# Performance work log

Measured on AMD Instinct MI355X. Metric: run time of the kernel, lower is better.

The kernel has to match this reference:

```python
import math
import jax, jax.numpy as jnp
import numpy as np

N_HEADS = 16
HIDDEN = 1024
FACTOR = 256
N_DK = HIDDEN // N_HEADS
B, S = 4, 2048


def _linear_params(key, fan_in, fan_out):
    kw, kb = jax.random.split(key)
    bound = 1.0 / math.sqrt(fan_in)
    W = jax.random.uniform(kw, (fan_in, fan_out), jnp.float32, -bound, bound)
    b = jax.random.uniform(kb, (fan_out,), jnp.float32, -bound, bound)
    return W, b


def setup_inputs() -> dict:
    key = jax.random.key(0)
    ks = jax.random.split(key, 12)
    inp = {
        "query": jax.random.normal(ks[0], (B, S, HIDDEN), jnp.float32),
        "key": jax.random.normal(ks[1], (B, S, HIDDEN), jnp.float32),
        "value": jax.random.normal(ks[2], (B, S, HIDDEN), jnp.float32),
        "mask": jax.random.randint(ks[3], (B, S), 0, 2, jnp.int32),
    }
    names = [("pq", HIDDEN, FACTOR), ("tq", FACTOR, HIDDEN),
             ("pk", HIDDEN, FACTOR), ("tk", FACTOR, HIDDEN),
             ("pv", HIDDEN, FACTOR), ("tv", FACTOR, HIDDEN),
             ("po", HIDDEN, FACTOR), ("to", FACTOR, HIDDEN)]
    for i, (nm, fi, fo) in enumerate(names):
        W, b = _linear_params(ks[4 + i], fi, fo)
        inp[f"W{nm}"], inp[f"b{nm}"] = W, b
    return inp


def _factored(x, Wp, bp, Wt, bt):
    # proj -> leaky_relu(0.2) -> tran
    h = jax.nn.leaky_relu(x @ Wp + bp, negative_slope=0.2)
    return h @ Wt + bt


def reference(query, key, value, mask,
              Wpq, bpq, Wtq, btq, Wpk, bpk, Wtk, btk,
              Wpv, bpv, Wtv, btv, Wpo, bpo, Wto, bto):
    bsize = query.shape[0]

    def split_heads(x):  # [B,S,H*Dk] -> [B,H,S,Dk]
        return x.reshape(bsize, -1, N_HEADS, N_DK).transpose(0, 2, 1, 3)

    q = split_heads(_factored(query, Wpq, bpq, Wtq, btq))
    k = split_heads(_factored(key, Wpk, bpk, Wtk, btk))
    v = split_heads(_factored(value, Wpv, bpv, Wtv, btv))

    scores = jnp.einsum("bhqd,bhkd->bhqk", q, k) / math.sqrt(N_DK)
    m = (mask == 0)[:, None, None, :]  # [B,1,1,S]
    scores = jnp.where(m, jnp.float32(-1e20), scores)
    attn = jax.nn.softmax(scores, axis=-1)
    cv = jnp.einsum("bhqk,bhkd->bhqd", attn, v)
    cv = cv.transpose(0, 2, 1, 3).reshape(bsize, -1, N_HEADS * N_DK)
    # dropout omitted (eval mode / deterministic reference)
    return _factored(cv, Wpo, bpo, Wto, bto)
```

## Files before the change

### kernel.cpp

```cpp
#include <hip/hip_runtime.h>
#include <cstdint>
#include <cstddef>

typedef __bf16 bf16_t;
typedef __bf16 bf16x8 __attribute__((ext_vector_type(8)));
typedef float  f32x4  __attribute__((ext_vector_type(4)));
typedef unsigned int uint32x4 __attribute__((ext_vector_type(4)));
typedef unsigned int uint32x2 __attribute__((ext_vector_type(2)));

#define DEV_INLINE __device__ __forceinline__

constexpr int Bsz = 4, Ssz = 2048, HID = 1024, FAC = 256, NH = 16, DKc = 64;
constexpr int Mrows = Bsz * Ssz;
constexpr float QSCALE = 0.18033688011112042f;

struct Ptr8 { const float* p[8]; };
struct Ptr3 { const float* p[3]; };

DEV_INLINE float fast_exp2(float x) {
#if __has_builtin(__builtin_amdgcn_exp2f)
  return __builtin_amdgcn_exp2f(x);
#else
  return exp2f(x);
#endif
}

DEV_INLINE void async16(const void* g, void* l) {
  __builtin_amdgcn_global_load_lds((const __attribute__((address_space(1))) void*)g,
                                   (__attribute__((address_space(3))) void*)l, 16, 0, 0);
}

#define WBAR(N) do { \
  asm volatile("s_waitcnt vmcnt(" #N ") lgkmcnt(0)" ::: "memory"); \
  __builtin_amdgcn_s_barrier(); \
} while (0)

DEV_INLINE int SW(int r) { return (r & 3) | ((r >> 1) & 4); }
DEV_INLINE int SW32(int r) { return (r >> 1) & 3; }

__global__ __launch_bounds__(256) void k_prep(Ptr8 w, Ptr8 bsrc, const int* __restrict__ mask,
                                              bf16_t* wpt, bf16_t* wtt,
                                              float* bp, float* bt, float* mf, bf16_t* mb) {
  const int z = blockIdx.z;
  if (z == 8) {
    if (blockIdx.x >= 64) return;
    const int i = blockIdx.x * 256 + threadIdx.x;
    if (i < 4 * FAC) bp[i] = bsrc.p[i >> 8][i & 255];
    if (i < 4 * HID) bt[i] = bsrc.p[4 + (i >> 10)][i & 1023];
    if (i < Bsz * Ssz) {
      const float m = (mask[i] != 0) ? 1.f : 0.f;
      mf[i] = m;
      mb[i] = (bf16_t)m;
    }
    return;
  }
  const int K = (z < 4) ? HID : FAC;
  const int N = (z < 4) ? FAC : HID;
  const int nbN = N / 32;
  const int nb = (blockIdx.x % nbN) * 32, kb = (blockIdx.x / nbN) * 32;
  __shared__ float t[32][33];
  const float* src = w.p[z];
  bf16_t* dst = (z < 4) ? (wpt + (size_t)z * FAC * HID) : (wtt + (size_t)(z - 4) * FAC * HID);
  const int tx = threadIdx.x & 31, ty = threadIdx.x >> 5;
#pragma unroll
  for (int j = 0; j < 4; ++j)
    t[ty + j * 8][tx] = src[(size_t)(kb + ty + j * 8) * N + nb + tx];
  __syncthreads();
#pragma unroll
  for (int j = 0; j < 4; ++j)
    dst[(size_t)(nb + ty + j * 8) * K + kb + tx] = (bf16_t)t[tx][ty + j * 8];
}

template <int CAST_A, int QKV, typename OUT_T>
__global__ __launch_bounds__(512, 2) void k_fact2(Ptr3 Asrc, const bf16_t* __restrict__ Abf,
                                                  const bf16_t* __restrict__ WpB,
                                                  const float* __restrict__ bpB,
                                                  const bf16_t* __restrict__ WtB,
                                                  const float* __restrict__ btB,
                                                  OUT_T* __restrict__ CoutAll,
                                                  bf16_t* __restrict__ C2,
                                                  const float* __restrict__ rowmul) {
  constexpr int LDTA = CAST_A ? 40 : 32;
  __shared__ __align__(16) bf16_t smem[128 * 264 + 4 * 256 * 32];
  bf16_t* As = smem;
  bf16_t* Hl = smem;
  bf16_t* Bs = smem + 128 * 264;

  const int z = QKV ? blockIdx.z : 0;
  const bf16_t* Wp = WpB + (size_t)z * FAC * HID;
  const float* bp = bpB + z * FAC;
  const bf16_t* Wt = WtB + (size_t)z * FAC * HID;
  const float* bt = btB + z * HID;
  OUT_T* Cout = QKV ? (CoutAll + (size_t)z * Mrows * HID) : CoutAll;

  const int tid = threadIdx.x;
  const int lane = tid & 63, wave = tid >> 6;
  const int quad = lane >> 4, l16 = lane & 15;
  const int swl = SW32(l16);
  const int m0 = blockIdx.x * 128;

  const int b1row = wave * 32 + (lane >> 2);
  const int bslot = (((lane & 3) ^ SW32(b1row)) & 3) * 8;
  const int wOff = wave * 1024;
  const bf16_t* gW0 = Wp + (size_t)b1row * HID + bslot;
  const bf16_t* gW1 = gW0 + (size_t)16 * HID;

  const int crow = tid >> 2, chalf = (tid & 3) * 8;
  const float* gAf = nullptr;
  const bf16_t* gAb = nullptr;
  if (CAST_A) {
    gAf = Asrc.p[z] + (size_t)(m0 + crow) * HID + chalf;
  } else {
    const int arowA = wave * 16 + (lane >> 2);
    const int aslot = (((lane & 3) ^ SW32(arowA)) & 3) * 8;
    gAb = Abf + (size_t)(m0 + arowA) * HID + aslot;
  }

#define STB1(t)                                              \
  do {                                                       \
    const int k0_ = (t) * 32;                                \
    bf16_t* d_ = Bs + ((t) & 3) * 8192 + wOff;               \
    async16(gW0 + k0_, d_);                                  \
    async16(gW1 + k0_, d_ + 512);                            \
  } while (0)
#define STA1(t) async16(gAb + (t) * 32, As + ((t) & 3) * 4096 + wave * 512)

  if (CAST_A) {
    f32x4 pa = *(const f32x4*)gAf;
    f32x4 pb = *(const f32x4*)(gAf + 4);
    __builtin_amdgcn_sched_barrier(0);
    STB1(0);
    STB1(1);
    union { bf16_t h[8]; uint32x4 u; } o;
#pragma unroll
    for (int j = 0; j < 4; ++j) { o.h[j] = (bf16_t)pa[j]; o.h[4 + j] = (bf16_t)pb[j]; }
    *(uint32x4*)(As + crow * LDTA + chalf) = o.u;
  } else {
    STA1(0); STB1(0);
    STA1(1); STB1(1);
  }

  f32x4 acc[8][2] = {};
  constexpr int nk = 32;

  for (int it = 0; it < nk; ++it) {
    if (CAST_A) {
      f32x4 xa, xb;
      const int k1 = (it + 1) * 32;
      if (it + 1 < nk) {
        xa = *(const f32x4*)(gAf + k1);
        xb = *(const f32x4*)(gAf + k1 + 4);
      }
      __builtin_amdgcn_sched_barrier(0);
      if (it + 2 < nk) STB1(it + 2);
      if (it + 2 < nk)      WBAR(6);
      else if (it + 1 < nk) WBAR(4);
      else                  WBAR(0);

      const bf16_t* Ac = As + (it % 3) * (128 * 40);
      const bf16_t* Bc = Bs + (it & 3) * 8192;
      bf16x8 af[8], bfr[2];
#pragma unroll
      for (int i = 0; i < 8; ++i)
        af[i] = *(const bf16x8*)(Ac + (i * 16 + l16) * LDTA + quad * 8);
#pragma unroll
      for (int i = 0; i < 2; ++i)
        bfr[i] = *(const bf16x8*)(Bc + (wave * 32 + i * 16 + l16) * 32 + ((quad ^ swl) & 3) * 8);
#pragma unroll
      for (int mi = 0; mi < 8; ++mi)
#pragma unroll
        for (int ni = 0; ni < 2; ++ni)
          acc[mi][ni] = __builtin_amdgcn_mfma_f32_16x16x32_bf16(af[mi], bfr[ni], acc[mi][ni], 0, 0, 0);

      if (it + 1 < nk) {
        union { bf16_t h[8]; uint32x4 u; } o;
#pragma unroll
        for (int j = 0; j < 4; ++j) { o.h[j] = (bf16_t)xa[j]; o.h[4 + j] = (bf16_t)xb[j]; }
        *(uint32x4*)(As + ((it + 1) % 3) * (128 * 40) + crow * LDTA + chalf) = o.u;
      }
    } else {
      if (it + 2 < nk) { STA1(it + 2); STB1(it + 2); }
      if (it + 2 < nk)      WBAR(6);
      else if (it + 1 < nk) WBAR(3);
      else                  WBAR(0);

      const bf16_t* Ac = As + (it & 3) * 4096;
      const bf16_t* Bc = Bs + (it & 3) * 8192;
      bf16x8 af[8], bfr[2];
#pragma unroll
      for (int i = 0; i < 8; ++i)
        af[i] = *(const bf16x8*)(Ac + (i * 16 + l16) * LDTA + ((quad ^ swl) & 3) * 8);
#pragma unroll
      for (int i = 0; i < 2; ++i)
        bfr[i] = *(const bf16x8*)(Bc + (wave * 32 + i * 16 + l16) * 32 + ((quad ^ swl) & 3) * 8);
#pragma unroll
      for (int mi = 0; mi < 8; ++mi)
#pragma unroll
        for (int ni = 0; ni < 2; ++ni)
          acc[mi][ni] = __builtin_amdgcn_mfma_f32_16x16x32_bf16(af[mi], bfr[ni], acc[mi][ni], 0, 0, 0);
    }
  }
#undef STA1

  __syncthreads();
#pragma unroll
  for (int mi = 0; mi < 8; ++mi)
#pragma unroll
    for (int ni = 0; ni < 2; ++ni) {
      const int col = wave * 32 + ni * 16 + l16;
      const float bv = bp[col];
#pragma unroll
      for (int r = 0; r < 4; ++r) {
        float y = acc[mi][ni][r] + bv;
        y = (y > 0.f) ? y : 0.2f * y;
        Hl[(mi * 16 + quad * 4 + r) * 264 + col] = (bf16_t)y;
      }
      acc[mi][ni] = (f32x4){0.f, 0.f, 0.f, 0.f};
    }
  __syncthreads();

#define STG2(ci)                                                              \
  do {                                                                        \
    const int nb_ = ((ci) >> 3) * 256, k0_ = ((ci) & 7) * 32;                 \
    const bf16_t* g_ = Wt + (size_t)(nb_ + b1row) * FAC + k0_ + bslot;        \
    bf16_t* d_ = Bs + ((ci) & 3) * 8192 + wOff;                               \
    async16(g_, d_);                                                          \
    async16(g_ + 16 * FAC, d_ + 512);                                         \
  } while (0)

  STG2(0);
  STG2(1);

  for (int ci = 0; ci < 32; ++ci) {
    if (ci + 2 < 32) STG2(ci + 2);
    if (ci + 2 < 32)      WBAR(4);
    else if (ci + 1 < 32) WBAR(2);
    else                  WBAR(0);

    const bf16_t* Bc = Bs + (ci & 3) * 8192;
    const int k0 = (ci & 7) * 32;
    bf16x8 af[8], bfr[2];
#pragma unroll
    for (int i = 0; i < 8; ++i)
      af[i] = *(const bf16x8*)(Hl + (i * 16 + l16) * 264 + k0 + quad * 8);
#pragma unroll
    for (int i = 0; i < 2; ++i)
      bfr[i] = *(const bf16x8*)(Bc + (wave * 32 + i * 16 + l16) * 32 + ((quad ^ swl) & 3) * 8);
#pragma unroll
    for (int mi = 0; mi < 8; ++mi)
#pragma unroll
      for (int ni = 0; ni < 2; ++ni)
        acc[mi][ni] = __builtin_amdgcn_mfma_f32_16x16x32_bf16(af[mi], bfr[ni], acc[mi][ni], 0, 0, 0);

    if ((ci & 7) == 7) {
      const int nbase = (ci >> 3) * 256;
      if (QKV && z == 2) {
#pragma unroll
        for (int mi = 0; mi < 8; ++mi) {
          const int rbase = m0 + mi * 16 + quad * 4;
          const int bb = rbase >> 11, s = rbase & 2047;
          float rmv[4];
#pragma unroll
          for (int r = 0; r < 4; ++r) rmv[r] = rowmul[rbase + r];
#pragma unroll
          for (int ni = 0; ni < 2; ++ni) {
            const int col = nbase + wave * 32 + ni * 16 + l16;
            const float bv = bt[col];
            const int hh = col >> 6, d = col & 63;
            union { bf16_t e[4]; uint32x2 u; } p;
#pragma unroll
            for (int r = 0; r < 4; ++r) p.e[r] = (bf16_t)((acc[mi][ni][r] + bv) * rmv[r]);
            *(uint32x2*)(C2 + (((size_t)((bb * NH + hh) * DKc + d)) << 11) + s) = p.u;
          }
        }
      } else {
        const float scale = (QKV && z == 0) ? QSCALE : 1.f;
#pragma unroll
        for (int mi = 0; mi < 8; ++mi) {
          const int row = m0 + mi * 16 + quad * 4;
#pragma unroll
          for (int ni = 0; ni < 2; ++ni) {
            const int col = nbase + wave * 32 + ni * 16 + l16;
            const float bv = bt[col];
#pragma unroll
            for (int r = 0; r < 4; ++r)
              Cout[(size_t)(row + r) * HID + col] = (OUT_T)((acc[mi][ni][r] + bv) * scale);
          }
        }
      }
#pragma unroll
      for (int mi = 0; mi < 8; ++mi)
#pragma unroll
        for (int ni = 0; ni < 2; ++ni) acc[mi][ni] = (f32x4){0.f, 0.f, 0.f, 0.f};
    }
  }
#undef STG2
#undef STB1
}

__global__ __launch_bounds__(512, 2) void k_attn(const bf16_t* __restrict__ qkv,
                                                 const bf16_t* __restrict__ mb,
                                                 bf16_t* __restrict__ cv) {
  __shared__ __align__(16) bf16_t Ks[4][64 * 64];
  __shared__ __align__(16) bf16_t Vt[4][64 * 64];
  __shared__ __align__(16) bf16_t Ml[Ssz];

  const int qt = blockIdx.x, h = blockIdx.y, b = blockIdx.z;
  const bf16_t* qp = qkv;
  const bf16_t* kp = qkv + (size_t)Mrows * HID;
  const bf16_t* vtp = qkv + 2 * (size_t)Mrows * HID + (size_t)(b * NH + h) * DKc * Ssz;

  const int tid = threadIdx.x;
  const int lane = tid & 63, wave = tid >> 6;
  const int quad = lane >> 4, l16 = lane & 15;

  const int r0 = wave * 8 + (lane >> 3);
  const int c0 = ((lane & 7) ^ SW(r0)) * 8;
  const int ldsOff = wave * 512;
  const bf16_t* kgA = kp + (size_t)(b * Ssz + r0) * HID + h * DKc + c0;
  const bf16_t* vgA = vtp + (size_t)r0 * Ssz + c0;

#define STAGEA(t, buf)                                          \
  do {                                                          \
    async16(kgA + (size_t)(t) * 64 * HID, Ks[buf] + ldsOff);    \
    async16(vgA + (t) * 64, Vt[buf] + ldsOff);                  \
  } while (0)

  *(uint32x2*)(Ml + tid * 4) = *(const uint32x2*)(mb + (size_t)b * Ssz + tid * 4);
  STAGEA(0, 0);
  STAGEA(1, 1);

  bf16x8 aq0[4], aq1[4];
#pragma unroll
  for (int g = 0; g < 4; ++g) {
    const size_t qrow = (size_t)(b * Ssz + qt * 512 + g * 128 + wave * 16 + l16) * HID + h * DKc + quad * 8;
    aq0[g] = *(const bf16x8*)(qp + qrow);
    aq1[g] = *(const bf16x8*)(qp + qrow + 32);
  }

  const int krow = 8 * (l16 >> 2) + (l16 & 3);
  f32x4 acc[4][4] = {};
  f32x4 dacc[4] = {};
  const bf16x8 zfrag = {};

  for (int kt = 0; kt < 32; ++kt) {
    if (kt + 2 < 32) STAGEA(kt + 2, (kt + 2) & 3);

    if (kt + 2 < 32)      WBAR(4);
    else if (kt + 1 < 32) WBAR(2);
    else                  WBAR(0);

    const bf16_t* Kc = Ks[kt & 3];
    const bf16_t* Vc = Vt[kt & 3];

    union U { uint32x4 u; bf16x8 h; } ap0[4], ap1[4];
    constexpr int koff[4] = {0, 4, 32, 36};
#pragma unroll
    for (int ks = 0; ks < 4; ++ks) {
      const int row = krow + koff[ks];
      const int sw = SW(row);
      bf16x8 a0 = *(const bf16x8*)(Kc + row * 64 + (quad ^ sw) * 8);
      bf16x8 a1 = *(const bf16x8*)(Kc + row * 64 + ((quad + 4) ^ sw) * 8);
#pragma unroll
      for (int g = 0; g < 4; ++g) {
        f32x4 c = {};
        c = __builtin_amdgcn_mfma_f32_16x16x32_bf16(a0, aq0[g], c, 0, 0, 0);
        c = __builtin_amdgcn_mfma_f32_16x16x32_bf16(a1, aq1[g], c, 0, 0, 0);
        union { bf16_t h[2]; uint32_t u; } p01, p23;
        p01.h[0] = (bf16_t)fast_exp2(c[0]);
        p01.h[1] = (bf16_t)fast_exp2(c[1]);
        p23.h[0] = (bf16_t)fast_exp2(c[2]);
        p23.h[1] = (bf16_t)fast_exp2(c[3]);
        U& t = (ks < 2) ? ap0[g] : ap1[g];
        t.u[(ks & 1) * 2] = p01.u;
        t.u[(ks & 1) * 2 + 1] = p23.u;
      }
    }

    bf16x8 mr0 = *(const bf16x8*)(Ml + kt * 64 + quad * 8);
    bf16x8 mr1 = *(const bf16x8*)(Ml + kt * 64 + 32 + quad * 8);
    if (l16 != 0) { mr0 = zfrag; mr1 = zfrag; }
#pragma unroll
    for (int g = 0; g < 4; ++g) {
      dacc[g] = __builtin_amdgcn_mfma_f32_16x16x32_bf16(ap0[g].h, mr0, dacc[g], 0, 0, 0);
      dacc[g] = __builtin_amdgcn_mfma_f32_16x16x32_bf16(ap1[g].h, mr1, dacc[g], 0, 0, 0);
    }

#pragma unroll
    for (int d = 0; d < 4; ++d) {
      const int row = d * 16 + l16;
      const int sw = SW(row);
      bf16x8 bv0 = *(const bf16x8*)(Vc + row * 64 + (quad ^ sw) * 8);
      bf16x8 bv1 = *(const bf16x8*)(Vc + row * 64 + ((quad + 4) ^ sw) * 8);
#pragma unroll
      for (int g = 0; g < 4; ++g) {
        acc[g][d] = __builtin_amdgcn_mfma_f32_16x16x32_bf16(ap0[g].h, bv0, acc[g][d], 0, 0, 0);
        acc[g][d] = __builtin_amdgcn_mfma_f32_16x16x32_bf16(ap1[g].h, bv1, acc[g][d], 0, 0, 0);
      }
    }
  }
#undef STAGEA

#pragma unroll
  for (int g = 0; g < 4; ++g) {
    const size_t obase = (size_t)(b * Ssz + qt * 512 + g * 128 + wave * 16 + quad * 4) * HID + h * DKc + l16;
#pragma unroll
    for (int r = 0; r < 4; ++r) {
      const float denom = __shfl(dacc[g][r], lane & 48, 64);
      const float rl = 1.f / denom;
#pragma unroll
      for (int d = 0; d < 4; ++d)
        cv[obase + (size_t)r * HID + d * 16] = (bf16_t)(acc[g][d][r] * rl);
    }
  }
}

extern "C" void kernel_launch(void* const* d_in, const int* in_sizes, int n_in,
                              void* d_out, int out_size, void* d_ws, size_t ws_size,
                              hipStream_t stream) {
  (void)in_sizes; (void)n_in; (void)out_size; (void)ws_size;
  const float* q_in = (const float*)d_in[0];
  const float* k_in = (const float*)d_in[1];
  const float* v_in = (const float*)d_in[2];
  const int* mask = (const int*)d_in[3];

  bf16_t* XB = (bf16_t*)d_ws;
  bf16_t* H3 = XB + (size_t)3 * Mrows * HID;
  bf16_t* CV = H3 + (size_t)3 * Mrows * FAC;
  bf16_t* WPT = CV + (size_t)Mrows * HID;
  bf16_t* WTT = WPT + (size_t)4 * FAC * HID;
  float* BP = (float*)(WTT + (size_t)4 * FAC * HID);
  float* BT = BP + 4 * FAC;
  float* MF = BT + 4 * HID;
  bf16_t* MB = (bf16_t*)(MF + Mrows);
  bf16_t* VTg = XB + 2 * (size_t)Mrows * HID;

  Ptr8 w;
  w.p[0] = (const float*)d_in[4];  w.p[1] = (const float*)d_in[8];
  w.p[2] = (const float*)d_in[12]; w.p[3] = (const float*)d_in[16];
  w.p[4] = (const float*)d_in[6];  w.p[5] = (const float*)d_in[10];
  w.p[6] = (const float*)d_in[14]; w.p[7] = (const float*)d_in[18];
  Ptr8 bs;
  bs.p[0] = (const float*)d_in[5];  bs.p[1] = (const float*)d_in[9];
  bs.p[2] = (const float*)d_in[13]; bs.p[3] = (const float*)d_in[17];
  bs.p[4] = (const float*)d_in[7];  bs.p[5] = (const float*)d_in[11];
  bs.p[6] = (const float*)d_in[15]; bs.p[7] = (const float*)d_in[19];
  hipLaunchKernelGGL(k_prep, dim3(256, 1, 9), dim3(256), 0, stream, w, bs, mask,
                     WPT, WTT, BP, BT, MF, MB);

  Ptr3 xs; xs.p[0] = q_in; xs.p[1] = k_in; xs.p[2] = v_in;
  Ptr3 nullp; nullp.p[0] = nullp.p[1] = nullp.p[2] = nullptr;

  hipLaunchKernelGGL((k_fact2<1, 1, bf16_t>), dim3(Mrows / 128, 1, 3), dim3(512), 0, stream,
                     xs, (const bf16_t*)nullptr, WPT, BP, WTT, BT, XB, VTg, MF);

  hipLaunchKernelGGL(k_attn, dim3(Ssz / 512, NH, Bsz), dim3(512), 0, stream, XB, MB, CV);

  hipLaunchKernelGGL((k_fact2<0, 0, float>), dim3(Mrows / 128, 1, 1), dim3(512), 0, stream,
                     nullp, CV, WPT + (size_t)3 * FAC * HID, BP + 3 * FAC,
                     WTT + (size_t)3 * FAC * HID, BT + 3 * HID,
                     (float*)d_out, (bf16_t*)nullptr, (const float*)nullptr);
}
```

Measured before the change: 332.8 us.

## Load GEMM A operand straight into registers and drop block barriers

The factored-linear kernel no longer stages the A tile through LDS. Each wave loads its full 128-row A slice from global memory into registers, with the fp32-to-bf16 cast done in registers, and prefetches the next k-step. The B tiles are per-wave LDS slices, so the workgroup barriers in both GEMM stages become plain vmcnt waits. This removes LDS round trips and s_barrier stalls. In exchange, all 8 waves read the same A data from global memory, which is 8x redundant traffic leaning on cache, and register pressure rises a lot under launch bounds (512,2).

```diff
diff --git a/kernel.cpp b/kernel.cpp
--- a/kernel.cpp
+++ b/kernel.cpp
@@ -29,6 +29,11 @@
   __builtin_amdgcn_global_load_lds((const __attribute__((address_space(1))) void*)g,
                                    (__attribute__((address_space(3))) void*)l, 16, 0, 0);
 }
+
+#define VWAIT(N) do { \
+  asm volatile("s_waitcnt vmcnt(" #N ")" ::: "memory"); \
+  __builtin_amdgcn_sched_barrier(0); \
+} while (0)
 
 #define WBAR(N) do { \
   asm volatile("s_waitcnt vmcnt(" #N ") lgkmcnt(0)" ::: "memory"); \
@@ -72,7 +77,7 @@
 }
 
 template <int CAST_A, int QKV, typename OUT_T>
-__global__ __launch_bounds__(512, 2) void k_fact2(Ptr3 Asrc, const bf16_t* __restrict__ Abf,
+__global__ __launch_bounds__(512, 2) void k_fact3(Ptr3 Asrc, const bf16_t* __restrict__ Abf,
                                                   const bf16_t* __restrict__ WpB,
                                                   const float* __restrict__ bpB,
                                                   const bf16_t* __restrict__ WtB,
@@ -80,11 +85,8 @@
                                                   OUT_T* __restrict__ CoutAll,
                                                   bf16_t* __restrict__ C2,
                                                   const float* __restrict__ rowmul) {
-  constexpr int LDTA = CAST_A ? 40 : 32;
-  __shared__ __align__(16) bf16_t smem[128 * 264 + 4 * 256 * 32];
-  bf16_t* As = smem;
-  bf16_t* Hl = smem;
-  bf16_t* Bs = smem + 128 * 264;
+  __shared__ __align__(16) bf16_t Hl[128 * 264];
+  __shared__ __align__(16) bf16_t Bs[4 * 256 * 32];
 
   const int z = QKV ? blockIdx.z : 0;
   const bf16_t* Wp = WpB + (size_t)z * FAC * HID;
@@ -105,16 +107,10 @@
   const bf16_t* gW0 = Wp + (size_t)b1row * HID + bslot;
   const bf16_t* gW1 = gW0 + (size_t)16 * HID;
 
-  const int crow = tid >> 2, chalf = (tid & 3) * 8;
   const float* gAf = nullptr;
-  const bf16_t* gAb = nullptr;
-  if (CAST_A) {
-    gAf = Asrc.p[z] + (size_t)(m0 + crow) * HID + chalf;
-  } else {
-    const int arowA = wave * 16 + (lane >> 2);
-    const int aslot = (((lane & 3) ^ SW32(arowA)) & 3) * 8;
-    gAb = Abf + (size_t)(m0 + arowA) * HID + aslot;
-  }
+  const bf16_t* gAb2 = nullptr;
+  if (CAST_A) gAf = Asrc.p[z] + (size_t)(m0 + l16) * HID + quad * 8;
+  else        gAb2 = Abf + (size_t)(m0 + l16) * HID + quad * 8;
 
 #define STB1(t)                                              \
   do {                                                       \
@@ -123,86 +119,75 @@
     async16(gW0 + k0_, d_);                                  \
     async16(gW1 + k0_, d_ + 512);                            \
   } while (0)
-#define STA1(t) async16(gAb + (t) * 32, As + ((t) & 3) * 4096 + wave * 512)
-
+
+  f32x4 fa[8], fb[8];
+  bf16x8 afC[8], afN[8];
   if (CAST_A) {
-    f32x4 pa = *(const f32x4*)gAf;
-    f32x4 pb = *(const f32x4*)(gAf + 4);
-    __builtin_amdgcn_sched_barrier(0);
-    STB1(0);
-    STB1(1);
-    union { bf16_t h[8]; uint32x4 u; } o;
-#pragma unroll
-    for (int j = 0; j < 4; ++j) { o.h[j] = (bf16_t)pa[j]; o.h[4 + j] = (bf16_t)pb[j]; }
-    *(uint32x4*)(As + crow * LDTA + chalf) = o.u;
+#pragma unroll
+    for (int mi = 0; mi < 8; ++mi) {
+      fa[mi] = *(const f32x4*)(gAf + (size_t)mi * 16 * HID);
+      fb[mi] = *(const f32x4*)(gAf + (size_t)mi * 16 * HID + 4);
+    }
   } else {
-    STA1(0); STB1(0);
-    STA1(1); STB1(1);
-  }
+#pragma unroll
+    for (int mi = 0; mi < 8; ++mi)
+      afC[mi] = *(const bf16x8*)(gAb2 + (size_t)mi * 16 * HID);
+  }
+  STB1(0);
+  STB1(1);
 
   f32x4 acc[8][2] = {};
   constexpr int nk = 32;
 
+#pragma unroll 2
   for (int it = 0; it < nk; ++it) {
     if (CAST_A) {
-      f32x4 xa, xb;
-      const int k1 = (it + 1) * 32;
+#pragma unroll
+      for (int mi = 0; mi < 8; ++mi) {
+        union { bf16_t h[8]; uint32x4 u; } o;
+#pragma unroll
+        for (int j = 0; j < 4; ++j) { o.h[j] = (bf16_t)fa[mi][j]; o.h[4 + j] = (bf16_t)fb[mi][j]; }
+        afC[mi] = *(bf16x8*)&o.u;
+      }
       if (it + 1 < nk) {
-        xa = *(const f32x4*)(gAf + k1);
-        xb = *(const f32x4*)(gAf + k1 + 4);
-      }
-      __builtin_amdgcn_sched_barrier(0);
+        const int k1 = (it + 1) * 32;
+#pragma unroll
+        for (int mi = 0; mi < 8; ++mi) {
+          fa[mi] = *(const f32x4*)(gAf + (size_t)mi * 16 * HID + k1);
+          fb[mi] = *(const f32x4*)(gAf + (size_t)mi * 16 * HID + k1 + 4);
+        }
+      }
       if (it + 2 < nk) STB1(it + 2);
-      if (it + 2 < nk)      WBAR(6);
-      else if (it + 1 < nk) WBAR(4);
-      else                  WBAR(0);
-
-      const bf16_t* Ac = As + (it % 3) * (128 * 40);
-      const bf16_t* Bc = Bs + (it & 3) * 8192;
-      bf16x8 af[8], bfr[2];
-#pragma unroll
-      for (int i = 0; i < 8; ++i)
-        af[i] = *(const bf16x8*)(Ac + (i * 16 + l16) * LDTA + quad * 8);
-#pragma unroll
-      for (int i = 0; i < 2; ++i)
-        bfr[i] = *(const bf16x8*)(Bc + (wave * 32 + i * 16 + l16) * 32 + ((quad ^ swl) & 3) * 8);
-#pragma unroll
-      for (int mi = 0; mi < 8; ++mi)
-#pragma unroll
-        for (int ni = 0; ni < 2; ++ni)
-          acc[mi][ni] = __builtin_amdgcn_mfma_f32_16x16x32_bf16(af[mi], bfr[ni], acc[mi][ni], 0, 0, 0);
-
+      VWAIT(18);
+    } else {
       if (it + 1 < nk) {
-        union { bf16_t h[8]; uint32x4 u; } o;
-#pragma unroll
-        for (int j = 0; j < 4; ++j) { o.h[j] = (bf16_t)xa[j]; o.h[4 + j] = (bf16_t)xb[j]; }
-        *(uint32x4*)(As + ((it + 1) % 3) * (128 * 40) + crow * LDTA + chalf) = o.u;
-      }
-    } else {
-      if (it + 2 < nk) { STA1(it + 2); STB1(it + 2); }
-      if (it + 2 < nk)      WBAR(6);
-      else if (it + 1 < nk) WBAR(3);
-      else                  WBAR(0);
-
-      const bf16_t* Ac = As + (it & 3) * 4096;
-      const bf16_t* Bc = Bs + (it & 3) * 8192;
-      bf16x8 af[8], bfr[2];
-#pragma unroll
-      for (int i = 0; i < 8; ++i)
-        af[i] = *(const bf16x8*)(Ac + (i * 16 + l16) * LDTA + ((quad ^ swl) & 3) * 8);
-#pragma unroll
-      for (int i = 0; i < 2; ++i)
-        bfr[i] = *(const bf16x8*)(Bc + (wave * 32 + i * 16 + l16) * 32 + ((quad ^ swl) & 3) * 8);
-#pragma unroll
-      for (int mi = 0; mi < 8; ++mi)
-#pragma unroll
-        for (int ni = 0; ni < 2; ++ni)
-          acc[mi][ni] = __builtin_amdgcn_mfma_f32_16x16x32_bf16(af[mi], bfr[ni], acc[mi][ni], 0, 0, 0);
-    }
-  }
-#undef STA1
-
-  __syncthreads();
+        const int k1 = (it + 1) * 32;
+#pragma unroll
+        for (int mi = 0; mi < 8; ++mi)
+          afN[mi] = *(const bf16x8*)(gAb2 + (size_t)mi * 16 * HID + k1);
+      }
+      if (it + 2 < nk) STB1(it + 2);
+      if (it + 1 < nk) VWAIT(10);
+      else             VWAIT(0);
+    }
+
+    const bf16_t* Bc = Bs + (it & 3) * 8192;
+    bf16x8 bfr[2];
+#pragma unroll
+    for (int i = 0; i < 2; ++i)
+      bfr[i] = *(const bf16x8*)(Bc + (wave * 32 + i * 16 + l16) * 32 + ((quad ^ swl) & 3) * 8);
+#pragma unroll
+    for (int mi = 0; mi < 8; ++mi)
+#pragma unroll
+      for (int ni = 0; ni < 2; ++ni)
+        acc[mi][ni] = __builtin_amdgcn_mfma_f32_16x16x32_bf16(afC[mi], bfr[ni], acc[mi][ni], 0, 0, 0);
+
+    if (!CAST_A && it + 1 < nk) {
+#pragma unroll
+      for (int mi = 0; mi < 8; ++mi) afC[mi] = afN[mi];
+    }
+  }
+
 #pragma unroll
   for (int mi = 0; mi < 8; ++mi)
 #pragma unroll
@@ -233,9 +218,9 @@
 
   for (int ci = 0; ci < 32; ++ci) {
     if (ci + 2 < 32) STG2(ci + 2);
-    if (ci + 2 < 32)      WBAR(4);
-    else if (ci + 1 < 32) WBAR(2);
-    else                  WBAR(0);
+    if (ci + 2 < 32)      VWAIT(4);
+    else if (ci + 1 < 32) VWAIT(2);
+    else                  VWAIT(0);
 
     const bf16_t* Bc = Bs + (ci & 3) * 8192;
     const int k0 = (ci & 7) * 32;
@@ -451,12 +436,12 @@
   Ptr3 xs; xs.p[0] = q_in; xs.p[1] = k_in; xs.p[2] = v_in;
   Ptr3 nullp; nullp.p[0] = nullp.p[1] = nullp.p[2] = nullptr;
 
-  hipLaunchKernelGGL((k_fact2<1, 1, bf16_t>), dim3(Mrows / 128, 1, 3), dim3(512), 0, stream,
+  hipLaunchKernelGGL((k_fact3<1, 1, bf16_t>), dim3(Mrows / 128, 1, 3), dim3(512), 0, stream,
                      xs, (const bf16_t*)nullptr, WPT, BP, WTT, BT, XB, VTg, MF);
 
   hipLaunchKernelGGL(k_attn, dim3(Ssz / 512, NH, Bsz), dim3(512), 0, stream, XB, MB, CV);
 
-  hipLaunchKernelGGL((k_fact2<0, 0, float>), dim3(Mrows / 128, 1, 1), dim3(512), 0, stream,
+  hipLaunchKernelGGL((k_fact3<0, 0, float>), dim3(Mrows / 128, 1, 1), dim3(512), 0, stream,
                      nullp, CV, WPT + (size_t)3 * FAC * HID, BP + 3 * FAC,
                      WTT + (size_t)3 * FAC * HID, BT + 3 * HID,
                      (float*)d_out, (bf16_t*)nullptr, (const float*)nullptr);
```

After: 456.1 us. 37.1% more time.
